# Kernel tuning notes

Hardware: AMD Instinct MI355X
Metric: run time of the kernel (lower is better)

Reference implementation:

```python
import jax, jax.numpy as jnp
import numpy as np

D_MODEL = 1024
H = 16
D_K = D_MODEL // H
NEG = -1.0e9


def setup_inputs() -> dict:
    key = jax.random.key(0)
    ks = jax.random.split(key, 12)
    B, S = 2, 2048
    s = 1.0 / np.sqrt(D_MODEL)
    inp = {
        "q": jax.random.normal(ks[0], (B, S, D_MODEL), jnp.float32),
        "k": jax.random.normal(ks[1], (B, S, D_MODEL), jnp.float32),
        "v": jax.random.normal(ks[2], (B, S, D_MODEL), jnp.float32),
        "mask": jnp.tril(jnp.ones((S, S), jnp.int32))[None, None, :, :],
        "wq": jax.random.normal(ks[3], (D_MODEL, D_MODEL), jnp.float32) * s,
        "bq": jax.random.normal(ks[4], (D_MODEL,), jnp.float32) * s,
        "wk": jax.random.normal(ks[5], (D_MODEL, D_MODEL), jnp.float32) * s,
        "bk": jax.random.normal(ks[6], (D_MODEL,), jnp.float32) * s,
        "wv": jax.random.normal(ks[7], (D_MODEL, D_MODEL), jnp.float32) * s,
        "bv": jax.random.normal(ks[8], (D_MODEL,), jnp.float32) * s,
        "wo": jax.random.normal(ks[9], (D_MODEL, D_MODEL), jnp.float32) * s,
        "bo": jax.random.normal(ks[10], (D_MODEL,), jnp.float32) * s,
    }
    return inp


def _split_heads(x):
    # [B,S,D] -> [B,H,S,d_k]
    B, S, _ = x.shape
    return x.reshape(B, S, H, D_K).transpose(0, 2, 1, 3)


def reference(q, k, v, mask, wq, bq, wk, bk, wv, bv, wo, bo):
    # torch Linear: y = x @ W.T + b
    query = _split_heads(q @ wq.T + bq)
    key = _split_heads(k @ wk.T + bk)
    value = _split_heads(v @ wv.T + bv)
    # scores: [B,H,S,S]
    scores = jnp.einsum("bhqd,bhkd->bhqk", query, key) / jnp.sqrt(
        jnp.asarray(D_K, query.dtype))
    scores = jnp.where(mask == 0, jnp.asarray(NEG, scores.dtype), scores)
    attn = jax.nn.softmax(scores, axis=-1)  # dropout p=0.0 -> identity
    x = jnp.einsum("bhqk,bhkd->bhqd", attn, value)
    B, _, S, _ = x.shape
    x = x.transpose(0, 2, 1, 3).reshape(B, S, D_MODEL)
    return x @ wo.T + bo
```

## Files before the change

kernel.cpp:

```cpp
#include <hip/hip_runtime.h>
#include <hip/hip_bf16.h>
#include <cstdint>
#include <cstddef>

#define BATCH 2
#define SEQ   2048
#define DM    1024
#define NH    16
#define DK    64
#define MROWS (BATCH*SEQ)

typedef __bf16 bf16;
typedef float  f32x4  __attribute__((ext_vector_type(4)));
typedef bf16   bf16x8 __attribute__((ext_vector_type(8)));
typedef bf16   bf16x4 __attribute__((ext_vector_type(4)));

#define MFMA32(a, b, c) __builtin_amdgcn_mfma_f32_16x16x32_bf16(a, b, c, 0, 0, 0)

__device__ __forceinline__ void llds16(const void* gc, void* l) {
    void* g = (void*)gc;
    __builtin_amdgcn_global_load_lds(
        (__attribute__((address_space(1))) uint32_t*)g,
        (__attribute__((address_space(3))) uint32_t*)l,
        16, 0, 0);
}

__global__ __launch_bounds__(256) void k_convert(
    const float* __restrict__ q, const float* __restrict__ k, const float* __restrict__ v,
    const float* __restrict__ wq, const float* __restrict__ wk, const float* __restrict__ wv,
    const float* __restrict__ wo,
    bf16* __restrict__ qb, bf16* __restrict__ kb, bf16* __restrict__ vb,
    bf16* __restrict__ wqb, bf16* __restrict__ wkb, bf16* __restrict__ wvb,
    bf16* __restrict__ wob) {
    long t = (long)blockIdx.x * blockDim.x + threadIdx.x;
    const long NQ = (long)MROWS * DM / 4;
    const long NW = (long)DM * DM / 4;
    const float* src; bf16* dst; long off;
    if (t < NQ)            { src = q;  dst = qb;  off = t; }
    else if (t < 2*NQ)     { src = k;  dst = kb;  off = t - NQ; }
    else if (t < 3*NQ)     { src = v;  dst = vb;  off = t - 2*NQ; }
    else {
        long u = t - 3*NQ;
        if (u < NW)        { src = wq; dst = wqb; off = u; }
        else if (u < 2*NW) { src = wk; dst = wkb; off = u - NW; }
        else if (u < 3*NW) { src = wv; dst = wvb; off = u - 2*NW; }
        else               { src = wo; dst = wob; off = u - 3*NW; }
    }
    f32x4 x = *(const f32x4*)(src + off * 4);
    bf16x4 y;
    y[0] = (bf16)x[0]; y[1] = (bf16)x[1]; y[2] = (bf16)x[2]; y[3] = (bf16)x[3];
    *(bf16x4*)(dst + off * 4) = y;
}

__global__ __launch_bounds__(512, 8) void k_gemm_qkv(
    const bf16* __restrict__ qb, const bf16* __restrict__ kb, const bf16* __restrict__ vb,
    const bf16* __restrict__ wqb, const bf16* __restrict__ wkb, const bf16* __restrict__ wvb,
    const float* __restrict__ bq, const float* __restrict__ bk, const float* __restrict__ bv,
    bf16* __restrict__ Qf, bf16* __restrict__ Kf, bf16* __restrict__ Vf) {
    const int z = blockIdx.z;
    const int bid = blockIdx.x;
    const bf16* A; const bf16* B; const float* bias;
    int m0, n0;
    if (z == 2) {
        A = vb; B = wvb; bias = bv;
        m0 = (bid >> 4) * 128;
        n0 = (bid & 15) * 64;
    } else {
        A = z ? wkb : wqb; B = z ? kb : qb; bias = z ? bk : bq;
        m0 = (bid >> 6) * 128;
        n0 = (bid & 63) * 64;
    }

    constexpr int K = DM, BK = 64;
    __shared__ bf16 sA[128 * BK];
    __shared__ bf16 sB[64 * BK];
    const int tid = threadIdx.x;
    const int l = tid & 63, w = tid >> 6;
    const int quad = l >> 4, l15 = l & 15;
    const int wm = w & 1, wn = w >> 1;
    const int srow = l >> 3;
    const int scol = ((l & 7) ^ srow) * 8;

    f32x4 acc[4] = {};
    for (int k0 = 0; k0 < K; k0 += BK) {
#pragma unroll
        for (int i = 0; i < 2; ++i) {
            int g8 = (w * 2 + i) * 8;
            llds16(A + (size_t)(m0 + g8 + srow) * K + k0 + scol, &sA[g8 * BK]);
        }
        {
            int g8 = w * 8;
            llds16(B + (size_t)(n0 + g8 + srow) * K + k0 + scol, &sB[g8 * BK]);
        }
        __syncthreads();

#pragma unroll
        for (int kk = 0; kk < 2; ++kk) {
            bf16x8 af[4], bfr;
            {
                int row = wn * 16 + l15;
                int byt = (row * 128 + kk * 64 + quad * 16) ^ ((row & 7) << 4);
                bfr = *(const bf16x8*)((const char*)sB + byt);
            }
#pragma unroll
            for (int mi = 0; mi < 4; ++mi) {
                int row = wm * 64 + mi * 16 + l15;
                int byt = (row * 128 + kk * 64 + quad * 16) ^ ((row & 7) << 4);
                af[mi] = *(const bf16x8*)((const char*)sA + byt);
            }
#pragma unroll
            for (int mi = 0; mi < 4; ++mi)
                acc[mi] = MFMA32(af[mi], bfr, acc[mi]);
        }
        __syncthreads();
    }

    if (z == 2) {
        int dcol = n0 + wn * 16 + l15;
        int hh2 = dcol >> 6;
        int dtile = (dcol >> 4) & 3;
        float bias_v = bias[dcol];
#pragma unroll
        for (int mi = 0; mi < 4; ++mi) {
            int srw = m0 + wm * 64 + mi * 16;
            int bb = srw >> 11, sl = srw & 2047;
            int kc = sl >> 5;
            bf16x4 pack;
#pragma unroll
            for (int r = 0; r < 4; ++r)
                pack[r] = (bf16)(acc[mi][r] + bias_v);
            size_t entry = ((size_t)(bb * NH + hh2) * 64 + kc) * 4 + dtile;
            *(bf16x4*)(Vf + entry * 512 + (size_t)(quad * 16 + l15) * 8 + (mi & 1) * 4) = pack;
        }
    } else {
        bf16* out = z ? Kf : Qf;
        const float scale = z ? 1.0f : 0.18033688f;
        int scolg = n0 + wn * 16 + l15;
        int bb = scolg >> 11, s = scolg & 2047;
        int s16 = s >> 4;
#pragma unroll
        for (int mi = 0; mi < 4; ++mi) {
            int drow = m0 + wm * 64 + mi * 16;
            int hh2 = (drow >> 6) & 15;
            int chunk = (drow & 63) >> 5;
            int qp = 2 * (mi & 1) + (quad >> 1);
            bf16x4 pack;
#pragma unroll
            for (int r = 0; r < 4; ++r)
                pack[r] = (bf16)((acc[mi][r] + bias[drow + quad * 4 + r]) * scale);
            size_t entry = ((size_t)(bb * NH + hh2) * 128 + s16) * 2 + chunk;
            *(bf16x4*)(out + entry * 512 + (size_t)(qp * 16 + l15) * 8 + (quad & 1) * 4) = pack;
        }
    }
}

__global__ __launch_bounds__(512, 4) void k_gemm_out(
    const bf16* __restrict__ X, const bf16* __restrict__ wob,
    const float* __restrict__ bo, float* __restrict__ out) {
    constexpr int K = DM, BK = 64, NS = K / BK;
    const int m0 = blockIdx.y * 128, n0 = blockIdx.x * 64;
    __shared__ bf16 sA[2][128 * BK];
    __shared__ bf16 sB[2][64 * BK];
    const int tid = threadIdx.x;
    const int l = tid & 63, w = tid >> 6;
    const int quad = l >> 4, l15 = l & 15;
    const int wm = w & 1, wn = w >> 1;
    const int srow = l >> 3;
    const int scol = ((l & 7) ^ srow) * 8;

#pragma unroll
    for (int i = 0; i < 2; ++i) {
        int g8 = (w * 2 + i) * 8;
        llds16(X + (size_t)(m0 + g8 + srow) * K + scol, &sA[0][g8 * BK]);
    }
    llds16(wob + (size_t)(n0 + w * 8 + srow) * K + scol, &sB[0][(w * 8) * BK]);

    f32x4 acc[4] = {};
    for (int s = 0; s < NS; ++s) {
        __syncthreads();
        const int cur = s & 1;
        if (s + 1 < NS) {
            const int k0 = (s + 1) * BK;
#pragma unroll
            for (int i = 0; i < 2; ++i) {
                int g8 = (w * 2 + i) * 8;
                llds16(X + (size_t)(m0 + g8 + srow) * K + k0 + scol, &sA[cur ^ 1][g8 * BK]);
            }
            llds16(wob + (size_t)(n0 + w * 8 + srow) * K + k0 + scol, &sB[cur ^ 1][(w * 8) * BK]);
        }

#pragma unroll
        for (int kk = 0; kk < 2; ++kk) {
            bf16x8 af[4], bfr;
            {
                int row = wn * 16 + l15;
                int byt = (row * 128 + kk * 64 + quad * 16) ^ ((row & 7) << 4);
                bfr = *(const bf16x8*)((const char*)&sB[cur][0] + byt);
            }
#pragma unroll
            for (int mi = 0; mi < 4; ++mi) {
                int row = wm * 64 + mi * 16 + l15;
                int byt = (row * 128 + kk * 64 + quad * 16) ^ ((row & 7) << 4);
                af[mi] = *(const bf16x8*)((const char*)&sA[cur][0] + byt);
            }
#pragma unroll
            for (int mi = 0; mi < 4; ++mi)
                acc[mi] = MFMA32(af[mi], bfr, acc[mi]);
        }
    }
    {
        int col = n0 + wn * 16 + l15;
        float bias_v = bo[col];
#pragma unroll
        for (int mi = 0; mi < 4; ++mi) {
            int rbase = m0 + wm * 64 + mi * 16 + quad * 4;
#pragma unroll
            for (int r = 0; r < 4; ++r)
                out[(size_t)(rbase + r) * DM + col] = acc[mi][r] + bias_v;
        }
    }
}

__global__ __launch_bounds__(256, 4) void k_flash(const bf16* __restrict__ Qf,
                                                  const bf16* __restrict__ Kf,
                                                  const bf16* __restrict__ Vf,
                                                  bf16* __restrict__ X) {
    const int bh = blockIdx.x;
    const int qt = 31 - (int)blockIdx.y;
    const int b = bh >> 4, h = bh & 15;
    const int tid = threadIdx.x, w = tid >> 6, l = tid & 63;
    const int quad = l >> 4, l15 = l & 15;
    __shared__ bf16 sKV[2][16 * 512];

    const bf16* qfp = Qf + (size_t)bh * 128 * 1024;
    const bf16* kfp = Kf + (size_t)bh * 128 * 1024;
    const bf16* vfp = Vf + (size_t)bh * 64 * 4 * 512;

    const int qt16 = qt * 4 + w;
    const int qglob = qt16 * 16 + l15;

    bf16x8 qf[2];
#pragma unroll
    for (int c = 0; c < 2; ++c)
        qf[c] = *(const bf16x8*)(qfp + ((size_t)qt16 * 2 + c) * 512 + (size_t)l * 8);

    f32x4 o[4] = {};
    float lp = 0.f;

#pragma unroll
    for (int i = 0; i < 4; ++i) {
        int e = w * 4 + i;
        const bf16* src = (e < 8) ? kfp + ((size_t)e) * 512
                                  : vfp + ((size_t)(e - 8)) * 512;
        llds16(src + (size_t)l * 8, &sKV[0][e * 512]);
    }

    for (int j = 0; j <= qt; ++j) {
        __syncthreads();
        const bf16* cur = sKV[j & 1];
        if (j < qt) {
            int j1 = j + 1;
#pragma unroll
            for (int i = 0; i < 4; ++i) {
                int e = w * 4 + i;
                const bf16* src = (e < 8) ? kfp + ((size_t)(j1 * 8 + e)) * 512
                                          : vfp + ((size_t)(j1 * 8 + (e - 8))) * 512;
                llds16(src + (size_t)l * 8, (void*)&sKV[j1 & 1][e * 512]);
            }
        }

        f32x4 st[4];
        __builtin_amdgcn_s_setprio(1);
#pragma unroll
        for (int ni = 0; ni < 4; ++ni) {
            bf16x8 k0 = *(const bf16x8*)&cur[(size_t)(ni * 2 + 0) * 512 + l * 8];
            bf16x8 k1 = *(const bf16x8*)&cur[(size_t)(ni * 2 + 1) * 512 + l * 8];
            f32x4 zz = {};
            zz = MFMA32(k0, qf[0], zz);
            st[ni] = MFMA32(k1, qf[1], zz);
        }
        __builtin_amdgcn_s_setprio(0);

        const bool diag = (j == qt);
#pragma unroll
        for (int c = 0; c < 2; ++c) {
            bf16x8 pb;
#pragma unroll
            for (int half = 0; half < 2; ++half) {
                int ni = 2 * c + half;
#pragma unroll
                for (int r = 0; r < 4; ++r) {
                    float s = st[ni][r];
                    if (diag) {
                        int key = j * 64 + ni * 16 + quad * 4 + r;
                        if (key > qglob) s = -1e30f;
                    }
                    float e = __builtin_amdgcn_exp2f(s);
                    lp += e;
                    pb[half * 4 + r] = (bf16)e;
                }
            }
            __builtin_amdgcn_s_setprio(1);
#pragma unroll
            for (int dt = 0; dt < 4; ++dt) {
                bf16x8 vv = *(const bf16x8*)&cur[(size_t)(8 + c * 4 + dt) * 512 + l * 8];
                o[dt] = MFMA32(vv, pb, o[dt]);
            }
            __builtin_amdgcn_s_setprio(0);
        }
    }

    lp += __shfl_xor(lp, 16, 64);
    lp += __shfl_xor(lp, 32, 64);
    float rv = 1.f / lp;

    __syncthreads();
    bf16* Xw = &sKV[0][w * 16 * 72];
#pragma unroll
    for (int dt = 0; dt < 4; ++dt) {
        bf16x4 pk;
#pragma unroll
        for (int r = 0; r < 4; ++r)
            pk[r] = (bf16)(o[dt][r] * rv);
        *(bf16x4*)&Xw[l15 * 72 + dt * 16 + quad * 4] = pk;
    }
#pragma unroll
    for (int i = 0; i < 2; ++i) {
        int row = i * 8 + (l >> 3);
        bf16x8 vv = *(const bf16x8*)&Xw[row * 72 + (l & 7) * 8];
        *(bf16x8*)(X + (size_t)(b * SEQ + qt16 * 16 + row) * DM + h * 64 + (l & 7) * 8) = vv;
    }
}

extern "C" void kernel_launch(void* const* d_in, const int* in_sizes, int n_in,
                              void* d_out, int out_size, void* d_ws, size_t ws_size,
                              hipStream_t stream) {
    const float* q  = (const float*)d_in[0];
    const float* k  = (const float*)d_in[1];
    const float* v  = (const float*)d_in[2];
    const float* wq = (const float*)d_in[4];
    const float* bq = (const float*)d_in[5];
    const float* wk = (const float*)d_in[6];
    const float* bk = (const float*)d_in[7];
    const float* wv = (const float*)d_in[8];
    const float* bv = (const float*)d_in[9];
    const float* wo = (const float*)d_in[10];
    const float* bo = (const float*)d_in[11];
    float* out = (float*)d_out;

    uint8_t* ws = (uint8_t*)d_ws;
    const size_t SZ_ACT = (size_t)MROWS * DM * sizeof(bf16);
    const size_t SZ_W   = (size_t)DM * DM * sizeof(bf16);
    bf16* qb  = (bf16*)(ws);
    bf16* kb  = (bf16*)(ws + SZ_ACT);
    bf16* vb  = (bf16*)(ws + 2 * SZ_ACT);
    bf16* wqb = (bf16*)(ws + 3 * SZ_ACT);
    bf16* wkb = (bf16*)(ws + 3 * SZ_ACT + SZ_W);
    bf16* wvb = (bf16*)(ws + 3 * SZ_ACT + 2 * SZ_W);
    bf16* wob = (bf16*)(ws + 3 * SZ_ACT + 3 * SZ_W);
    bf16* Qf  = (bf16*)(ws + 3 * SZ_ACT + 4 * SZ_W);
    bf16* Kf  = (bf16*)(ws + 4 * SZ_ACT + 4 * SZ_W);
    bf16* Vf  = (bf16*)(ws + 5 * SZ_ACT + 4 * SZ_W);
    bf16* X   = (bf16*)(ws + 6 * SZ_ACT + 4 * SZ_W);

    {
        long total_vec4 = 3L * MROWS * DM / 4 + 4L * DM * DM / 4;
        k_convert<<<dim3((unsigned)(total_vec4 / 256)), 256, 0, stream>>>(
            q, k, v, wq, wk, wv, wo, qb, kb, vb, wqb, wkb, wvb, wob);
    }
    k_gemm_qkv<<<dim3(512, 1, 3), 512, 0, stream>>>(
        qb, kb, vb, wqb, wkb, wvb, bq, bk, bv, Qf, Kf, Vf);
    k_flash<<<dim3(BATCH * NH, SEQ / 64), 256, 0, stream>>>(Qf, Kf, Vf, X);
    k_gemm_out<<<dim3(DM / 64, MROWS / 128), 512, 0, stream>>>(X, wob, bo, out);
}
```

Before: 208.0 us.

## Fuse fp32-to-bf16 activation conversion into QKV projection GEMM tile loads

The separate conversion pass over the q, k and v activations is removed. The QKV GEMM now reads fp32 activations straight from global memory, converts them to bf16 in registers, and writes them into the swizzled LDS tile. Weights are still converted by a smaller kernel. This saves a full write and read of the bf16 activation copies, but activation staging now goes through registers with synchronous loads instead of direct global-to-LDS loads, and each activation tile is re-read from fp32 by several blocks.

```diff
diff --git a/kernel.cpp b/kernel.cpp
--- a/kernel.cpp
+++ b/kernel.cpp
@@ -25,27 +25,29 @@
         16, 0, 0);
 }
 
-__global__ __launch_bounds__(256) void k_convert(
-    const float* __restrict__ q, const float* __restrict__ k, const float* __restrict__ v,
-    const float* __restrict__ wq, const float* __restrict__ wk, const float* __restrict__ wv,
-    const float* __restrict__ wo,
-    bf16* __restrict__ qb, bf16* __restrict__ kb, bf16* __restrict__ vb,
-    bf16* __restrict__ wqb, bf16* __restrict__ wkb, bf16* __restrict__ wvb,
-    bf16* __restrict__ wob) {
+__device__ __forceinline__ void stage_f32row(const float* srcRow, bf16* ldsTile,
+                                             int rowLocal, int slot) {
+    const f32x4 a = *(const f32x4*)(srcRow + slot * 8);
+    const f32x4 c = *(const f32x4*)(srcRow + slot * 8 + 4);
+    bf16x8 v;
+    v[0] = (bf16)a[0]; v[1] = (bf16)a[1]; v[2] = (bf16)a[2]; v[3] = (bf16)a[3];
+    v[4] = (bf16)c[0]; v[5] = (bf16)c[1]; v[6] = (bf16)c[2]; v[7] = (bf16)c[3];
+    int byt = (rowLocal * 128 + slot * 16) ^ ((rowLocal & 7) << 4);
+    *(bf16x8*)((char*)ldsTile + byt) = v;
+}
+
+__global__ __launch_bounds__(256) void k_convert_w(
+    const float* __restrict__ wq, const float* __restrict__ wk,
+    const float* __restrict__ wv, const float* __restrict__ wo,
+    bf16* __restrict__ wqb, bf16* __restrict__ wkb,
+    bf16* __restrict__ wvb, bf16* __restrict__ wob) {
     long t = (long)blockIdx.x * blockDim.x + threadIdx.x;
-    const long NQ = (long)MROWS * DM / 4;
     const long NW = (long)DM * DM / 4;
     const float* src; bf16* dst; long off;
-    if (t < NQ)            { src = q;  dst = qb;  off = t; }
-    else if (t < 2*NQ)     { src = k;  dst = kb;  off = t - NQ; }
-    else if (t < 3*NQ)     { src = v;  dst = vb;  off = t - 2*NQ; }
-    else {
-        long u = t - 3*NQ;
-        if (u < NW)        { src = wq; dst = wqb; off = u; }
-        else if (u < 2*NW) { src = wk; dst = wkb; off = u - NW; }
-        else if (u < 3*NW) { src = wv; dst = wvb; off = u - 2*NW; }
-        else               { src = wo; dst = wob; off = u - 3*NW; }
-    }
+    if (t < NW)            { src = wq; dst = wqb; off = t; }
+    else if (t < 2*NW)     { src = wk; dst = wkb; off = t - NW; }
+    else if (t < 3*NW)     { src = wv; dst = wvb; off = t - 2*NW; }
+    else                   { src = wo; dst = wob; off = t - 3*NW; }
     f32x4 x = *(const f32x4*)(src + off * 4);
     bf16x4 y;
     y[0] = (bf16)x[0]; y[1] = (bf16)x[1]; y[2] = (bf16)x[2]; y[3] = (bf16)x[3];
@@ -53,20 +55,20 @@
 }
 
 __global__ __launch_bounds__(512, 8) void k_gemm_qkv(
-    const bf16* __restrict__ qb, const bf16* __restrict__ kb, const bf16* __restrict__ vb,
+    const float* __restrict__ qf32, const float* __restrict__ kf32, const float* __restrict__ vf32,
     const bf16* __restrict__ wqb, const bf16* __restrict__ wkb, const bf16* __restrict__ wvb,
     const float* __restrict__ bq, const float* __restrict__ bk, const float* __restrict__ bv,
     bf16* __restrict__ Qf, bf16* __restrict__ Kf, bf16* __restrict__ Vf) {
     const int z = blockIdx.z;
     const int bid = blockIdx.x;
-    const bf16* A; const bf16* B; const float* bias;
+    const bf16* W; const float* ACT; const float* bias;
     int m0, n0;
     if (z == 2) {
-        A = vb; B = wvb; bias = bv;
+        ACT = vf32; W = wvb; bias = bv;
         m0 = (bid >> 4) * 128;
         n0 = (bid & 15) * 64;
     } else {
-        A = z ? wkb : wqb; B = z ? kb : qb; bias = z ? bk : bq;
+        W = z ? wkb : wqb; ACT = z ? kf32 : qf32; bias = z ? bk : bq;
         m0 = (bid >> 6) * 128;
         n0 = (bid & 63) * 64;
     }
@@ -80,17 +82,25 @@
     const int wm = w & 1, wn = w >> 1;
     const int srow = l >> 3;
     const int scol = ((l & 7) ^ srow) * 8;
+    const int slot = l & 7;
 
     f32x4 acc[4] = {};
     for (int k0 = 0; k0 < K; k0 += BK) {
-#pragma unroll
-        for (int i = 0; i < 2; ++i) {
-            int g8 = (w * 2 + i) * 8;
-            llds16(A + (size_t)(m0 + g8 + srow) * K + k0 + scol, &sA[g8 * BK]);
-        }
-        {
-            int g8 = w * 8;
-            llds16(B + (size_t)(n0 + g8 + srow) * K + k0 + scol, &sB[g8 * BK]);
+        if (z == 2) {
+#pragma unroll
+            for (int i = 0; i < 2; ++i) {
+                int rowLocal = (w * 2 + i) * 8 + srow;
+                stage_f32row(ACT + (size_t)(m0 + rowLocal) * K + k0, sA, rowLocal, slot);
+            }
+            llds16(W + (size_t)(n0 + w * 8 + srow) * K + k0 + scol, &sB[(w * 8) * BK]);
+        } else {
+#pragma unroll
+            for (int i = 0; i < 2; ++i) {
+                int g8 = (w * 2 + i) * 8;
+                llds16(W + (size_t)(m0 + g8 + srow) * K + k0 + scol, &sA[g8 * BK]);
+            }
+            int rowLocal = w * 8 + srow;
+            stage_f32row(ACT + (size_t)(n0 + rowLocal) * K + k0, sB, rowLocal, slot);
         }
         __syncthreads();
 
@@ -351,25 +361,19 @@
     uint8_t* ws = (uint8_t*)d_ws;
     const size_t SZ_ACT = (size_t)MROWS * DM * sizeof(bf16);
     const size_t SZ_W   = (size_t)DM * DM * sizeof(bf16);
-    bf16* qb  = (bf16*)(ws);
-    bf16* kb  = (bf16*)(ws + SZ_ACT);
-    bf16* vb  = (bf16*)(ws + 2 * SZ_ACT);
-    bf16* wqb = (bf16*)(ws + 3 * SZ_ACT);
-    bf16* wkb = (bf16*)(ws + 3 * SZ_ACT + SZ_W);
-    bf16* wvb = (bf16*)(ws + 3 * SZ_ACT + 2 * SZ_W);
-    bf16* wob = (bf16*)(ws + 3 * SZ_ACT + 3 * SZ_W);
-    bf16* Qf  = (bf16*)(ws + 3 * SZ_ACT + 4 * SZ_W);
-    bf16* Kf  = (bf16*)(ws + 4 * SZ_ACT + 4 * SZ_W);
-    bf16* Vf  = (bf16*)(ws + 5 * SZ_ACT + 4 * SZ_W);
-    bf16* X   = (bf16*)(ws + 6 * SZ_ACT + 4 * SZ_W);
-
-    {
-        long total_vec4 = 3L * MROWS * DM / 4 + 4L * DM * DM / 4;
-        k_convert<<<dim3((unsigned)(total_vec4 / 256)), 256, 0, stream>>>(
-            q, k, v, wq, wk, wv, wo, qb, kb, vb, wqb, wkb, wvb, wob);
-    }
+    bf16* wqb = (bf16*)(ws);
+    bf16* wkb = (bf16*)(ws + SZ_W);
+    bf16* wvb = (bf16*)(ws + 2 * SZ_W);
+    bf16* wob = (bf16*)(ws + 3 * SZ_W);
+    bf16* Qf  = (bf16*)(ws + 4 * SZ_W);
+    bf16* Kf  = (bf16*)(ws + 4 * SZ_W + SZ_ACT);
+    bf16* Vf  = (bf16*)(ws + 4 * SZ_W + 2 * SZ_ACT);
+    bf16* X   = (bf16*)(ws + 4 * SZ_W + 3 * SZ_ACT);
+
+    k_convert_w<<<dim3(4 * DM * DM / 4 / 256), 256, 0, stream>>>(
+        wq, wk, wv, wo, wqb, wkb, wvb, wob);
     k_gemm_qkv<<<dim3(512, 1, 3), 512, 0, stream>>>(
-        qb, kb, vb, wqb, wkb, wvb, bq, bk, bv, Qf, Kf, Vf);
+        q, k, v, wqb, wkb, wvb, bq, bk, bv, Qf, Kf, Vf);
     k_flash<<<dim3(BATCH * NH, SEQ / 64), 256, 0, stream>>>(Qf, Kf, Vf, X);
     k_gemm_out<<<dim3(DM / 64, MROWS / 128), 512, 0, stream>>>(X, wob, bo, out);
 }
```

Measured after the change: 222.1 us. 6.8% more time.
